# Kernel optimization log

Hardware: AMD Instinct MI355X
Metric: run time of the kernel (lower is better)

## Reference

```python
import math
import jax, jax.numpy as jnp
import numpy as np

WIDTH = 512
F_TOT = 1024          # min(2*width, 2048)
F_CHUNK = 128
RHO = 0.25
SPECTRAL_SCALE = 0.8
ES_BETA = 6.0
TAU = 0.001
EPS = 1e-8
LN_EPS = 1e-5
N_TOKENS = 4096


def setup_inputs() -> dict:
    key = jax.random.key(0)
    ks = jax.random.split(key, 4)
    x = jax.random.normal(ks[0], (N_TOKENS, WIDTH), dtype=jnp.float32)
    # freq init: linspace(-pi, pi, F) repeated across width
    freq = jnp.tile(jnp.linspace(-math.pi, math.pi, F_TOT, dtype=jnp.float32)[:, None], (1, WIDTH))
    alpha = jax.random.normal(ks[1], (F_TOT, WIDTH), dtype=jnp.float32) * 0.01
    gate = jnp.ones((F_TOT, WIDTH), dtype=jnp.float32) * 0.01
    ln_gamma = jnp.ones((WIDTH,), dtype=jnp.float32)
    ln_beta = jnp.zeros((WIDTH,), dtype=jnp.float32)
    # torch Linear default init: U(-1/sqrt(in), 1/sqrt(in))
    bound = 1.0 / math.sqrt(WIDTH)
    w_loc = jax.random.uniform(ks[2], (WIDTH, WIDTH), dtype=jnp.float32, minval=-bound, maxval=bound)
    b_loc = jax.random.uniform(ks[3], (WIDTH,), dtype=jnp.float32, minval=-bound, maxval=bound)
    return {"x": x, "freq": freq, "alpha": alpha, "gate": gate,
            "ln_gamma": ln_gamma, "ln_beta": ln_beta, "w_loc": w_loc, "b_loc": b_loc}


def reference(x, freq, alpha, gate, ln_gamma, ln_beta, w_loc, b_loc):
    # LayerNorm
    mu = jnp.mean(x, axis=-1, keepdims=True)
    var = jnp.mean((x - mu) ** 2, axis=-1, keepdims=True)
    x_n = (x - mu) / jnp.sqrt(var + LN_EPS) * ln_gamma + ln_beta

    # local branch: Linear -> GELU (exact erf, torch default)
    h_local = jax.nn.gelu(x_n @ w_loc.T + b_loc, approximate=False)

    # spectral weights
    f = freq * SPECTRAL_SCALE
    denom = jax.lax.stop_gradient(jnp.max(jnp.abs(f)))  # .detach().abs().amax()
    safe = jnp.where(denom < 1e-8, 1.0, denom)
    win = jnp.where(denom < 1e-8, jnp.ones_like(f), jnp.exp(-ES_BETA * (f / safe) ** 2))
    raw = alpha * gate
    thr_w = jnp.sign(raw) * jax.nn.relu(jnp.abs(raw) - TAU) * win

    # chunked sin basis expansion, accumulated with lax.scan
    n_chunks = F_TOT // F_CHUNK
    f_r = f.reshape(n_chunks, F_CHUNK, WIDTH)
    t_r = thr_w.reshape(n_chunks, F_CHUNK, WIDTH)

    def body(acc, ft):
        fc, tc = ft  # [C, W] each
        basis = jnp.sin(x_n[:, None, :] * fc[None, :, :])  # [N, C, W]
        return acc + jnp.einsum('ncw,cw->nw', basis, tc), None

    h_spec, _ = jax.lax.scan(jax.checkpoint(body), jnp.zeros_like(x_n), (f_r, t_r))

    # RMS normalize over width
    rms = jnp.sqrt(jnp.mean(h_spec ** 2, axis=1, keepdims=True) + EPS)
    h_spec = h_spec / rms
    return h_local + RHO * h_spec
```

## Files before the change

kernel.cpp:

```cpp
#include <hip/hip_runtime.h>
#include <hip/hip_bf16.h>
#include <math.h>

#define N_TOK 4096
#define W 512
#define F_TOT 1024
#define FW (F_TOT * W)

#define OFF_PARTIAL 0
#define OFF_NNZ     1024
#define OFF_XN      4096
#define OFF_WB      4198400
#define OFF_E       4722688
#define OFF_T       6819840
#define OFF_C       8916992

typedef __attribute__((ext_vector_type(8))) short bf16x8;
typedef __attribute__((ext_vector_type(4))) float f32x4;

__global__ __launch_bounds__(256) void ln_prep(
    const float* __restrict__ x, const float* __restrict__ freq,
    const float* __restrict__ gamma, const float* __restrict__ beta,
    const float* __restrict__ wloc, __hip_bfloat16* __restrict__ xn,
    __hip_bfloat16* __restrict__ wb, float* __restrict__ partial,
    unsigned* __restrict__ nnz) {
  __shared__ float red[256];
  __shared__ float red2[256];
  const int n = blockIdx.x, t = threadIdx.x;
  const float v0 = x[n * W + t];
  const float v1 = x[n * W + t + 256];
  red[t] = v0 + v1;
  red2[t] = v0 * v0 + v1 * v1;
  __syncthreads();
  for (int s = 128; s > 0; s >>= 1) {
    if (t < s) { red[t] += red[t + s]; red2[t] += red2[t + s]; }
    __syncthreads();
  }
  const float mu = red[0] * (1.0f / W);
  const float var = red2[0] * (1.0f / W) - mu * mu;
  const float rstd = rsqrtf(var + 1e-5f);
  xn[n * W + t]       = __float2bfloat16((v0 - mu) * rstd * gamma[t] + beta[t]);
  xn[n * W + t + 256] = __float2bfloat16((v1 - mu) * rstd * gamma[t + 256] + beta[t + 256]);

  if (n < 256) {
    float m = 0.0f;
    const float* fp = freq + n * 2048;
#pragma unroll
    for (int j = 0; j < 8; ++j) m = fmaxf(m, fabsf(fp[t + j * 256]));
    __syncthreads();
    red[t] = m;
    __syncthreads();
    for (int s = 128; s > 0; s >>= 1) {
      if (t < s) red[t] = fmaxf(red[t], red[t + s]);
      __syncthreads();
    }
    if (t == 0) {
      partial[n] = red[0];
      if (n == 0) *nnz = 0u;
    }
  } else if (n >= 512 && n < 1536) {
    const int i = (n - 512) * 256 + t;
    wb[i] = __float2bfloat16(wloc[i]);
  }
}

__global__ __launch_bounds__(256) void thr_compact(
    const float* __restrict__ freq, const float* __restrict__ alpha,
    const float* __restrict__ gate, const float* __restrict__ partial,
    unsigned* __restrict__ nnz, unsigned* __restrict__ eArr,
    float* __restrict__ tArr, float* __restrict__ cArr) {
  __shared__ float red[256];
  const int t = threadIdx.x;
  red[t] = partial[t];
  __syncthreads();
  for (int s = 128; s > 0; s >>= 1) {
    if (t < s) red[t] = fmaxf(red[t], red[t + s]);
    __syncthreads();
  }
  const float denom = red[0] * 0.8f;
  const bool tiny = denom < 1e-8f;
  const float inv = tiny ? 0.0f : (1.0f / denom);
  const int base = blockIdx.x * 1024 + t;
#pragma unroll
  for (int j = 0; j < 4; ++j) {
    const int e = base + j * 256;
    const float f = freq[e] * 0.8f;
    const float raw = alpha[e] * gate[e];
    const float v = fabsf(raw) - 1e-3f;
    if (v > 0.0f) {
      const float r = f * inv;
      const float win = tiny ? 1.0f : expf(-6.0f * r * r);
      const float tw = copysignf(v, raw) * win;
      const unsigned idx = atomicAdd(nnz, 1u);
      eArr[idx] = (unsigned)e;
      tArr[idx] = tw;
      cArr[idx] = f;
    }
  }
}

__global__ __launch_bounds__(64) void gemm_gelu(
    const __hip_bfloat16* __restrict__ xn, const __hip_bfloat16* __restrict__ wb,
    const float* __restrict__ bias, float* __restrict__ out) {
  const int tm = blockIdx.x >> 3;
  const int tn = blockIdx.x & 7;
  const int lane = threadIdx.x;
  const int m = lane & 15;
  const int q = lane >> 4;
  const short* A = (const short*)xn + (tm * 64) * W;
  const short* B = (const short*)wb + (tn * 64) * W;
  f32x4 acc[4][4] = {};

  for (int k0 = 0; k0 < W; k0 += 32) {
    const int koff = k0 + q * 8;
    bf16x8 a[4], b[4];
#pragma unroll
    for (int i = 0; i < 4; ++i)
      a[i] = *(const bf16x8*)(A + (i * 16 + m) * W + koff);
#pragma unroll
    for (int j = 0; j < 4; ++j)
      b[j] = *(const bf16x8*)(B + (j * 16 + m) * W + koff);
#pragma unroll
    for (int i = 0; i < 4; ++i)
#pragma unroll
      for (int j = 0; j < 4; ++j)
        acc[i][j] = __builtin_amdgcn_mfma_f32_16x16x32_bf16(a[i], b[j], acc[i][j], 0, 0, 0);
  }

#pragma unroll
  for (int i = 0; i < 4; ++i) {
#pragma unroll
    for (int j = 0; j < 4; ++j) {
      const int col = tn * 64 + j * 16 + m;
      const float bv = bias[col];
#pragma unroll
      for (int r = 0; r < 4; ++r) {
        const int row = tm * 64 + i * 16 + q * 4 + r;
        const float v = acc[i][j][r] + bv;
        const float g = 0.5f * v * (1.0f + erff(v * 0.70710678118654752f));
        out[row * W + col] = g;
      }
    }
  }
}

__global__ __launch_bounds__(256) void spectral_final(
    const __hip_bfloat16* __restrict__ xn, const unsigned* __restrict__ nnz,
    const unsigned* __restrict__ eArr, const float* __restrict__ tArr,
    const float* __restrict__ cArr, float* __restrict__ out) {
  const unsigned cnt = *nnz;
  if (cnt == 0) return;
  __shared__ float red[256];
  const int t = threadIdx.x;
  for (int n = blockIdx.x; n < N_TOK; n += gridDim.x) {
    const int c0 = t, c1 = t + 256;
    const float x0 = __bfloat162float(xn[n * W + c0]);
    const float x1 = __bfloat162float(xn[n * W + c1]);
    float h0 = 0.0f, h1 = 0.0f;
    for (unsigned i = 0; i < cnt; ++i) {
      const unsigned e = eArr[i];
      const int we = (int)(e & (W - 1));
      const float tw = tArr[i];
      const float cf = cArr[i];
      if (we == c0) h0 += tw * sinf(x0 * cf);
      else if (we == c1) h1 += tw * sinf(x1 * cf);
    }
    red[t] = h0 * h0 + h1 * h1;
    __syncthreads();
    for (int s = 128; s > 0; s >>= 1) {
      if (t < s) red[t] += red[t + s];
      __syncthreads();
    }
    const float rms = sqrtf(red[0] * (1.0f / W) + 1e-8f);
    const float sc = 0.25f / rms;
    out[n * W + c0] += sc * h0;
    out[n * W + c1] += sc * h1;
    __syncthreads();
  }
}

extern "C" void kernel_launch(void* const* d_in, const int* in_sizes, int n_in,
                              void* d_out, int out_size, void* d_ws, size_t ws_size,
                              hipStream_t stream) {
  const float* x     = (const float*)d_in[0];
  const float* freq  = (const float*)d_in[1];
  const float* alpha = (const float*)d_in[2];
  const float* gate  = (const float*)d_in[3];
  const float* gamma = (const float*)d_in[4];
  const float* beta  = (const float*)d_in[5];
  const float* wloc  = (const float*)d_in[6];
  const float* bloc  = (const float*)d_in[7];
  float* out = (float*)d_out;

  char* ws = (char*)d_ws;
  float* partial       = (float*)(ws + OFF_PARTIAL);
  unsigned* nnz        = (unsigned*)(ws + OFF_NNZ);
  __hip_bfloat16* xn   = (__hip_bfloat16*)(ws + OFF_XN);
  __hip_bfloat16* wb   = (__hip_bfloat16*)(ws + OFF_WB);
  unsigned* eArr       = (unsigned*)(ws + OFF_E);
  float* tArr          = (float*)(ws + OFF_T);
  float* cArr          = (float*)(ws + OFF_C);

  hipLaunchKernelGGL(ln_prep, dim3(N_TOK), dim3(256), 0, stream,
                     x, freq, gamma, beta, wloc, xn, wb, partial, nnz);
  hipLaunchKernelGGL(thr_compact, dim3(512), dim3(256), 0, stream,
                     freq, alpha, gate, partial, nnz, eArr, tArr, cArr);
  hipLaunchKernelGGL(gemm_gelu, dim3(512), dim3(64), 0, stream,
                     xn, wb, bloc, out);
  hipLaunchKernelGGL(spectral_final, dim3(512), dim3(256), 0, stream,
                     xn, nnz, eArr, tArr, cArr, out);
}
```

Measured before the change: 103.4 us.

## Use wave-per-row LayerNorm and smaller register-prefetched GEMM tiles

LayerNorm now runs one wavefront per row with float4 loads and shuffle reductions instead of shared-memory tree reductions, cutting the prep grid from 4096 to 1536 blocks. The freq max and weight conversion paths are vectorized the same way, and the partial-max buffer grows to 1024 entries. The GEMM tile shrinks from 64x64 to 16x64 per wave, giving 4x more blocks, and prefetches the next K slice into registers. Occupancy and latency hiding should improve, but A/B reuse per wave drops, so global/L2 traffic rises.

After: 103.0 us. No clear change (-0.4%).

```diff
diff --git a/kernel.cpp b/kernel.cpp
--- a/kernel.cpp
+++ b/kernel.cpp
@@ -8,14 +8,15 @@
 #define FW (F_TOT * W)
 
 #define OFF_PARTIAL 0
-#define OFF_NNZ     1024
-#define OFF_XN      4096
-#define OFF_WB      4198400
-#define OFF_E       4722688
-#define OFF_T       6819840
-#define OFF_C       8916992
+#define OFF_NNZ     4096
+#define OFF_XN      8192
+#define OFF_WB      4202496
+#define OFF_E       4726784
+#define OFF_T       6823936
+#define OFF_C       8921088
 
 typedef __attribute__((ext_vector_type(8))) short bf16x8;
+typedef __attribute__((ext_vector_type(4))) short bf16x4;
 typedef __attribute__((ext_vector_type(4))) float f32x4;
 
 __global__ __launch_bounds__(256) void ln_prep(
@@ -24,43 +25,58 @@
     const float* __restrict__ wloc, __hip_bfloat16* __restrict__ xn,
     __hip_bfloat16* __restrict__ wb, float* __restrict__ partial,
     unsigned* __restrict__ nnz) {
-  __shared__ float red[256];
-  __shared__ float red2[256];
-  const int n = blockIdx.x, t = threadIdx.x;
-  const float v0 = x[n * W + t];
-  const float v1 = x[n * W + t + 256];
-  red[t] = v0 + v1;
-  red2[t] = v0 * v0 + v1 * v1;
-  __syncthreads();
-  for (int s = 128; s > 0; s >>= 1) {
-    if (t < s) { red[t] += red[t + s]; red2[t] += red2[t + s]; }
-    __syncthreads();
-  }
-  const float mu = red[0] * (1.0f / W);
-  const float var = red2[0] * (1.0f / W) - mu * mu;
-  const float rstd = rsqrtf(var + 1e-5f);
-  xn[n * W + t]       = __float2bfloat16((v0 - mu) * rstd * gamma[t] + beta[t]);
-  xn[n * W + t + 256] = __float2bfloat16((v1 - mu) * rstd * gamma[t + 256] + beta[t + 256]);
-
-  if (n < 256) {
-    float m = 0.0f;
-    const float* fp = freq + n * 2048;
-#pragma unroll
-    for (int j = 0; j < 8; ++j) m = fmaxf(m, fabsf(fp[t + j * 256]));
-    __syncthreads();
-    red[t] = m;
-    __syncthreads();
-    for (int s = 128; s > 0; s >>= 1) {
-      if (t < s) red[t] = fmaxf(red[t], red[t + s]);
-      __syncthreads();
-    }
-    if (t == 0) {
-      partial[n] = red[0];
-      if (n == 0) *nnz = 0u;
-    }
-  } else if (n >= 512 && n < 1536) {
-    const int i = (n - 512) * 256 + t;
-    wb[i] = __float2bfloat16(wloc[i]);
+  const int b = blockIdx.x, t = threadIdx.x;
+  const int wv = t >> 6, lane = t & 63;
+  if (b < 1024) {
+    const int row = b * 4 + wv;
+    const float4* xr = (const float4*)(x + row * W);
+    const float4 p0 = xr[lane * 2];
+    const float4 p1 = xr[lane * 2 + 1];
+    float s  = p0.x + p0.y + p0.z + p0.w + p1.x + p1.y + p1.z + p1.w;
+    float ss = p0.x*p0.x + p0.y*p0.y + p0.z*p0.z + p0.w*p0.w
+             + p1.x*p1.x + p1.y*p1.y + p1.z*p1.z + p1.w*p1.w;
+#pragma unroll
+    for (int m = 32; m > 0; m >>= 1) {
+      s  += __shfl_xor(s, m);
+      ss += __shfl_xor(ss, m);
+    }
+    const float mu = s * (1.0f / W);
+    const float var = ss * (1.0f / W) - mu * mu;
+    const float rstd = rsqrtf(var + 1e-5f);
+    const float4 g0 = ((const float4*)gamma)[lane * 2];
+    const float4 g1 = ((const float4*)gamma)[lane * 2 + 1];
+    const float4 be0 = ((const float4*)beta)[lane * 2];
+    const float4 be1 = ((const float4*)beta)[lane * 2 + 1];
+    alignas(16) __hip_bfloat16 o[8];
+    o[0] = __float2bfloat16((p0.x - mu) * rstd * g0.x + be0.x);
+    o[1] = __float2bfloat16((p0.y - mu) * rstd * g0.y + be0.y);
+    o[2] = __float2bfloat16((p0.z - mu) * rstd * g0.z + be0.z);
+    o[3] = __float2bfloat16((p0.w - mu) * rstd * g0.w + be0.w);
+    o[4] = __float2bfloat16((p1.x - mu) * rstd * g1.x + be1.x);
+    o[5] = __float2bfloat16((p1.y - mu) * rstd * g1.y + be1.y);
+    o[6] = __float2bfloat16((p1.z - mu) * rstd * g1.z + be1.z);
+    o[7] = __float2bfloat16((p1.w - mu) * rstd * g1.w + be1.w);
+    *(bf16x8*)(xn + row * W + lane * 8) = *(const bf16x8*)o;
+  } else if (b < 1280) {
+    const int b2 = b - 1024;
+    const float4* fp = (const float4*)(freq + b2 * 2048 + wv * 512);
+    const float4 q0 = fp[lane * 2];
+    const float4 q1 = fp[lane * 2 + 1];
+    float mx = fmaxf(fmaxf(fmaxf(fabsf(q0.x), fabsf(q0.y)), fmaxf(fabsf(q0.z), fabsf(q0.w))),
+                     fmaxf(fmaxf(fabsf(q1.x), fabsf(q1.y)), fmaxf(fabsf(q1.z), fabsf(q1.w))));
+#pragma unroll
+    for (int m = 32; m > 0; m >>= 1) mx = fmaxf(mx, __shfl_xor(mx, m));
+    if (lane == 0) partial[b2 * 4 + wv] = mx;
+    if (b == 1024 && t == 0) *nnz = 0u;
+  } else {
+    const int i4 = ((b - 1280) * 256 + t);
+    const float4 v = ((const float4*)wloc)[i4];
+    alignas(8) __hip_bfloat16 o[4];
+    o[0] = __float2bfloat16(v.x);
+    o[1] = __float2bfloat16(v.y);
+    o[2] = __float2bfloat16(v.z);
+    o[3] = __float2bfloat16(v.w);
+    *(bf16x4*)(wb + i4 * 4) = *(const bf16x4*)o;
   }
 }
 
@@ -71,7 +87,8 @@
     float* __restrict__ tArr, float* __restrict__ cArr) {
   __shared__ float red[256];
   const int t = threadIdx.x;
-  red[t] = partial[t];
+  red[t] = fmaxf(fmaxf(partial[t], partial[t + 256]),
+                 fmaxf(partial[t + 512], partial[t + 768]));
   __syncthreads();
   for (int s = 128; s > 0; s >>= 1) {
     if (t < s) red[t] = fmaxf(red[t], red[t + s]);
@@ -107,39 +124,43 @@
   const int lane = threadIdx.x;
   const int m = lane & 15;
   const int q = lane >> 4;
-  const short* A = (const short*)xn + (tm * 64) * W;
-  const short* B = (const short*)wb + (tn * 64) * W;
-  f32x4 acc[4][4] = {};
-
+  const short* A = (const short*)xn + (tm * 16 + m) * W + q * 8;
+  const short* B = (const short*)wb + (tn * 64 + m) * W + q * 8;
+  f32x4 acc[4] = {};
+
+  bf16x8 a_cur = *(const bf16x8*)A;
+  bf16x8 b_cur[4];
+#pragma unroll
+  for (int j = 0; j < 4; ++j) b_cur[j] = *(const bf16x8*)(B + (j * 16) * W);
+
+#pragma unroll
   for (int k0 = 0; k0 < W; k0 += 32) {
-    const int koff = k0 + q * 8;
-    bf16x8 a[4], b[4];
-#pragma unroll
-    for (int i = 0; i < 4; ++i)
-      a[i] = *(const bf16x8*)(A + (i * 16 + m) * W + koff);
+    bf16x8 a_nxt;
+    bf16x8 b_nxt[4];
+    if (k0 + 32 < W) {
+      a_nxt = *(const bf16x8*)(A + k0 + 32);
+#pragma unroll
+      for (int j = 0; j < 4; ++j)
+        b_nxt[j] = *(const bf16x8*)(B + (j * 16) * W + k0 + 32);
+    }
 #pragma unroll
     for (int j = 0; j < 4; ++j)
-      b[j] = *(const bf16x8*)(B + (j * 16 + m) * W + koff);
-#pragma unroll
-    for (int i = 0; i < 4; ++i)
-#pragma unroll
-      for (int j = 0; j < 4; ++j)
-        acc[i][j] = __builtin_amdgcn_mfma_f32_16x16x32_bf16(a[i], b[j], acc[i][j], 0, 0, 0);
-  }
-
-#pragma unroll
-  for (int i = 0; i < 4; ++i) {
-#pragma unroll
-    for (int j = 0; j < 4; ++j) {
-      const int col = tn * 64 + j * 16 + m;
-      const float bv = bias[col];
-#pragma unroll
-      for (int r = 0; r < 4; ++r) {
-        const int row = tm * 64 + i * 16 + q * 4 + r;
-        const float v = acc[i][j][r] + bv;
-        const float g = 0.5f * v * (1.0f + erff(v * 0.70710678118654752f));
-        out[row * W + col] = g;
-      }
+      acc[j] = __builtin_amdgcn_mfma_f32_16x16x32_bf16(a_cur, b_cur[j], acc[j], 0, 0, 0);
+    a_cur = a_nxt;
+#pragma unroll
+    for (int j = 0; j < 4; ++j) b_cur[j] = b_nxt[j];
+  }
+
+#pragma unroll
+  for (int j = 0; j < 4; ++j) {
+    const int col = tn * 64 + j * 16 + m;
+    const float bv = bias[col];
+#pragma unroll
+    for (int r = 0; r < 4; ++r) {
+      const int row = tm * 16 + q * 4 + r;
+      const float v = acc[j][r] + bv;
+      const float g = 0.5f * v * (1.0f + erff(v * 0.70710678118654752f));
+      out[row * W + col] = g;
     }
   }
 }
@@ -201,11 +222,11 @@
   float* tArr          = (float*)(ws + OFF_T);
   float* cArr          = (float*)(ws + OFF_C);
 
-  hipLaunchKernelGGL(ln_prep, dim3(N_TOK), dim3(256), 0, stream,
+  hipLaunchKernelGGL(ln_prep, dim3(1536), dim3(256), 0, stream,
                      x, freq, gamma, beta, wloc, xn, wb, partial, nnz);
   hipLaunchKernelGGL(thr_compact, dim3(512), dim3(256), 0, stream,
                      freq, alpha, gate, partial, nnz, eArr, tArr, cArr);
-  hipLaunchKernelGGL(gemm_gelu, dim3(512), dim3(64), 0, stream,
+  hipLaunchKernelGGL(gemm_gelu, dim3(2048), dim3(64), 0, stream,
                      xn, wb, bloc, out);
   hipLaunchKernelGGL(spectral_final, dim3(512), dim3(256), 0, stream,
                      xn, nnz, eArr, tArr, cArr, out);
```
